# Kernel tuning notes

Hardware: AMD Instinct MI355X
Metric: run time of the kernel (lower is better)

## Reference

```python
import jax, jax.numpy as jnp
import numpy as np

B, T, D, H, FFN = 2, 2048, 1024, 16, 4096
K = D // H
EPS = 1e-6      # denominator clamp (module eps)
LN_EPS = 1e-5   # torch LayerNorm default
LAM_MIN = 1e-8  # lam clamp before log (exp(log(clamp)) == clamp)


def setup_inputs() -> dict:
    key = jax.random.key(0)
    ks = jax.random.split(key, 12)
    s = 0.02
    w = lambda k, shp: (jax.random.normal(k, shp, jnp.float32) * s)
    return {
        "x": jax.random.normal(ks[0], (B, T, D), jnp.float32),
        "q_w": w(ks[1], (D, D)), "q_b": jnp.zeros((D,), jnp.float32),
        "k_w": w(ks[2], (D, D)), "k_b": jnp.zeros((D,), jnp.float32),
        "v_w": w(ks[3], (D, D)), "v_b": jnp.zeros((D,), jnp.float32),
        "o_w": w(ks[4], (D, D)), "o_b": jnp.zeros((D,), jnp.float32),
        "ln1_w": jnp.ones((D,), jnp.float32), "ln1_b": jnp.zeros((D,), jnp.float32),
        "ln2_w": jnp.ones((D,), jnp.float32), "ln2_b": jnp.zeros((D,), jnp.float32),
        "dec_w": w(ks[5], (D, H)), "dec_b": jnp.full((H,), 5.0, jnp.float32),
        "f1_w": w(ks[6], (D, FFN)), "f1_b": jnp.zeros((FFN,), jnp.float32),
        "f2_w": w(ks[7], (FFN, D)), "f2_b": jnp.zeros((D,), jnp.float32),
    }


def _ln(x, w, b):
    m = x.mean(-1, keepdims=True)
    v = ((x - m) ** 2).mean(-1, keepdims=True)
    return (x - m) * jax.lax.rsqrt(v + LN_EPS) * w + b


def _lion(phi_q, phi_k, v, lam):
    """Bidirectional selective-decay linear attention.
    out_i = sum_j prod_{t in (min(i,j), max(i,j)]} lam_t * (phi_q_i . phi_k_j) v_j
    phi_q, phi_k, lam: (B,H,T,K); v: (B,H,T,Kv). Returns (B,H,T,Kv).
    Implemented as a forward scan (j<=i) + reverse scan (j>i); diagonal counted once.
    """
    b, h, t, kk = phi_q.shape
    kv = v.shape[-1]
    to_t = lambda a: a.transpose(2, 0, 1, 3)  # (T,B,H,*)
    qt, kt, vt, lt = to_t(phi_q), to_t(phi_k), to_t(v), to_t(lam)
    S0 = jnp.zeros((b, h, kk, kv), phi_q.dtype)

    def fwd(S, inp):
        q_t, k_t, v_t, l_t = inp
        S = S * l_t[..., None] + k_t[..., None] * v_t[..., None, :]
        return S, jnp.einsum('bhk,bhkv->bhv', q_t, S)

    _, out_f = jax.lax.scan(fwd, S0, (qt, kt, vt, lt))  # (T,B,H,Kv)

    q_shift = jnp.concatenate([qt[:1], qt[:-1]], axis=0)  # query at t-1 paired with R_{t-1}

    def bwd(R, inp):
        qs_t, k_t, v_t, l_t = inp
        R = l_t[..., None] * (k_t[..., None] * v_t[..., None, :] + R)
        return R, jnp.einsum('bhk,bhkv->bhv', qs_t, R)

    _, out_b = jax.lax.scan(bwd, S0, (q_shift, kt, vt, lt), reverse=True)
    # out_b[t] = phi_q_{t-1} . R_{t-1}; query i gets out_b[i+1]; R_{T-1} = 0
    out_b = jnp.concatenate([out_b[1:], jnp.zeros_like(out_b[:1])], axis=0)
    return (out_f + out_b).transpose(1, 2, 0, 3)  # (B,H,T,Kv)


def reference(x, q_w, q_b, k_w, k_b, v_w, v_b, o_w, o_b,
              ln1_w, ln1_b, ln2_w, ln2_b, dec_w, dec_b,
              f1_w, f1_b, f2_w, f2_b):
    bb, tt, dd = x.shape
    residual = x
    x_n = _ln(x, ln1_w, ln1_b)

    split = lambda y: y.reshape(bb, tt, H, K).transpose(0, 2, 1, 3)  # (B,H,T,K)
    q = split(x_n @ q_w + q_b)
    k = split(x_n @ k_w + k_b)
    v = split(x_n @ v_w + v_b)
    phi_q = jax.nn.elu(q) + 1.0
    phi_k = jax.nn.elu(k) + 1.0

    # selective per-head decay, broadcast across K
    lam = jax.nn.sigmoid(x_n @ dec_w + dec_b)            # (B,T,H)
    lam = jnp.maximum(lam, LAM_MIN).transpose(0, 2, 1)   # (B,H,T)
    lam = jnp.broadcast_to(lam[..., None], (bb, H, tt, K))

    # v-extended trick: extra ones column yields the row-sum denominator
    v_ext = jnp.concatenate([v, jnp.ones((bb, H, tt, 1), v.dtype)], axis=-1)
    out = _lion(phi_q, phi_k, v_ext, lam)                # (B,H,T,K+1)
    num, den = out[..., :K], jnp.maximum(out[..., K:], EPS)
    attn = (num / den).transpose(0, 2, 1, 3).reshape(bb, tt, dd)

    x = residual + (attn @ o_w + o_b)
    x2 = _ln(x, ln2_w, ln2_b)
    h = jax.nn.gelu(x2 @ f1_w + f1_b, approximate=False)
    return x + (h @ f2_w + f2_b)
```

## Files before the change

### kernel.cpp

```cpp
#include <hip/hip_runtime.h>
#include <cstdint>

#define Bq 2
#define Tq 2048
#define Dq 1024
#define Hq 16
#define FFNq 4096
#define NCHUNK 32
#define ROWS (Bq*Tq)
#define STW 5120

typedef unsigned short u16;
typedef __attribute__((ext_vector_type(4))) float f32x4;

enum { ACT_NONE = 0, ACT_ELU1 = 1, ACT_GELU = 2 };

#define MFMA16(acc, a, b) \
  asm("v_mfma_f32_16x16x32_bf16 %0, %1, %2, %0" : "+v"(acc) : "v"(a), "v"(b))
#define VMWAIT(N) asm volatile("s_waitcnt vmcnt(" #N ")" ::: "memory")

__device__ __forceinline__ u16 f2bf(float f) {
  uint32_t u = __float_as_uint(f);
  uint32_t r = (u + 0x7FFFu + ((u >> 16) & 1u)) >> 16;
  return (u16)r;
}
__device__ __forceinline__ float bf2f(u16 u) {
  return __uint_as_float(((uint32_t)u) << 16);
}

__device__ __forceinline__ void gload16(const void* g, void* l) {
  __builtin_amdgcn_global_load_lds(
      (const __attribute__((address_space(1))) uint32_t*)g,
      (__attribute__((address_space(3))) uint32_t*)l, 16, 0, 0);
}

__device__ __forceinline__ void xcd_swizzle(int& bx, int& by) {
  const int gx = gridDim.x;
  const int nwg = gx * gridDim.y;
  int flat = by * gx + bx;
  flat = (flat & 7) * (nwg >> 3) + (flat >> 3);
  bx = flat % gx;
  by = flat / gx;
}

__global__ __launch_bounds__(256) void wconv_all(
    const float* __restrict__ q_w, const float* __restrict__ k_w,
    const float* __restrict__ v_w, const float* __restrict__ o_w,
    const float* __restrict__ f1_w, const float* __restrict__ f2_w,
    u16* __restrict__ qkvT, u16* __restrict__ owT,
    u16* __restrict__ f1T, u16* __restrict__ f2T)
{
  const int bid = blockIdx.x;
  const float* src; u16* dst; int Kd, N, bx, by;
  if (bid < 1024) {
    const int m = bid >> 8, t = bid & 255;
    src = (m == 0) ? q_w : (m == 1) ? k_w : (m == 2) ? v_w : o_w;
    dst = (m == 3) ? owT : qkvT + (size_t)m * 1024 * 1024;
    Kd = 1024; N = 1024; bx = t & 15; by = t >> 4;
  } else if (bid < 2048) {
    const int t = bid - 1024;
    src = f1_w; dst = f1T; Kd = 1024; N = 4096; bx = t & 63; by = t >> 6;
  } else {
    const int t = bid - 2048;
    src = f2_w; dst = f2T; Kd = 4096; N = 1024; bx = t & 15; by = t >> 4;
  }
  __shared__ float tb[64][65];
  const int n0 = bx * 64, k0 = by * 64;
  const int tid = threadIdx.x;
  #pragma unroll
  for (int r = 0; r < 4; ++r) {
    const int s = tid + r * 256;
    const int kk = s >> 4, nn = (s & 15) << 2;
    const float4 v = *(const float4*)(src + (size_t)(k0 + kk) * N + n0 + nn);
    tb[kk][nn] = v.x; tb[kk][nn+1] = v.y; tb[kk][nn+2] = v.z; tb[kk][nn+3] = v.w;
  }
  __syncthreads();
  const int n = tid >> 2;
  const int ks = (tid & 3) << 4;
  uint32_t pk[8];
  #pragma unroll
  for (int j = 0; j < 8; ++j) {
    const float a = tb[ks + 2*j][n];
    const float c = tb[ks + 2*j + 1][n];
    pk[j] = (uint32_t)f2bf(a) | ((uint32_t)f2bf(c) << 16);
  }
  u16* drow = dst + (size_t)(n0 + n) * Kd + k0 + ks;
  *(uint4*)(drow)     = make_uint4(pk[0], pk[1], pk[2], pk[3]);
  *(uint4*)(drow + 8) = make_uint4(pk[4], pk[5], pk[6], pk[7]);
}

__global__ __launch_bounds__(256) void ln_kernel(
    const float* __restrict__ x, const float* __restrict__ w,
    const float* __restrict__ b, u16* __restrict__ outb)
{
  const int row = blockIdx.x;
  const int tid = threadIdx.x;
  const float* xr = x + (size_t)row * Dq;
  float4 v = *(const float4*)(xr + tid * 4);
  float s  = v.x + v.y + v.z + v.w;
  float s2 = v.x*v.x + v.y*v.y + v.z*v.z + v.w*v.w;
  #pragma unroll
  for (int off = 32; off > 0; off >>= 1) {
    s  += __shfl_down(s,  off);
    s2 += __shfl_down(s2, off);
  }
  __shared__ float rs[4], rs2[4];
  const int wid = tid >> 6, lane = tid & 63;
  if (lane == 0) { rs[wid] = s; rs2[wid] = s2; }
  __syncthreads();
  const float ts  = rs[0] + rs[1] + rs[2] + rs[3];
  const float ts2 = rs2[0] + rs2[1] + rs2[2] + rs2[3];
  const float mean = ts * (1.f / Dq);
  const float var  = ts2 * (1.f / Dq) - mean * mean;
  const float rstd = rsqrtf(var + 1e-5f);
  const float4 wv = *(const float4*)(w + tid * 4);
  const float4 bv = *(const float4*)(b + tid * 4);
  float4 o;
  o.x = (v.x - mean) * rstd * wv.x + bv.x;
  o.y = (v.y - mean) * rstd * wv.y + bv.y;
  o.z = (v.z - mean) * rstd * wv.z + bv.z;
  o.w = (v.w - mean) * rstd * wv.w + bv.w;
  uint2 p;
  p.x = (uint32_t)f2bf(o.x) | ((uint32_t)f2bf(o.y) << 16);
  p.y = (uint32_t)f2bf(o.z) | ((uint32_t)f2bf(o.w) << 16);
  *(uint2*)(outb + (size_t)row * Dq + tid * 4) = p;
}

template<int BM, int BN, int TW, int WM, int WN, int NB, int ACT, bool RES, bool F32OUT, bool QKVMODE>
__global__ __launch_bounds__(TW) void mgemm(
    const u16* __restrict__ A, const u16* __restrict__ BT,
    const float* __restrict__ b0, const float* __restrict__ b1,
    const float* __restrict__ b2, const float* __restrict__ res,
    void* __restrict__ C0, void* __restrict__ C1, void* __restrict__ C2,
    int M, int N, int Kd)
{
  constexpr int GA = (BM * 32) / (TW * 8);
  constexpr int GB = (BN * 32) / (TW * 8);
  constexpr int L  = GA + GB;
  constexpr int MR = BM / WM / 16;
  constexpr int NR = BN / WN / 16;
  constexpr int VMAIN = (NB - 2) * L;
  __shared__ u16 As[NB][BM * 32];
  __shared__ u16 Bs[NB][BN * 32];
  const int tid = threadIdx.x;
  const int lane = tid & 63, wid = tid >> 6;
  const int wr = wid / WN, wc = wid % WN;
  int bx = blockIdx.x, by = blockIdx.y;
  xcd_swizzle(bx, by);
  const int rowBase = by * BM;
  const int colBase = bx * BN;

  f32x4 acc[MR][NR] = {};

  const int srow = tid >> 2;
  const int skb  = (((tid & 3) ^ ((tid >> 3) & 3)) << 3);
  const u16* ag[GA];
  const u16* bg[GB];
  #pragma unroll
  for (int g = 0; g < GA; ++g)
    ag[g] = A  + (size_t)(rowBase + g * (TW / 4) + srow) * Kd + skb;
  #pragma unroll
  for (int g = 0; g < GB; ++g)
    bg[g] = BT + (size_t)(colBase + g * (TW / 4) + srow) * Kd + skb;

  const int fr = lane & 15, fq = lane >> 4;
  const int rsw = (fq ^ ((fr >> 1) & 3)) * 8;

  auto STAGE = [&](int buf, int k0) {
    #pragma unroll
    for (int g = 0; g < GA; ++g) gload16(ag[g] + k0, &As[buf][(g * TW + tid) * 8]);
    #pragma unroll
    for (int g = 0; g < GB; ++g) gload16(bg[g] + k0, &Bs[buf][(g * TW + tid) * 8]);
  };

  const int NT = Kd >> 5;
  #pragma unroll
  for (int s = 0; s < NB - 1; ++s) STAGE(s, s << 5);
  int cur = 0, wbuf = NB - 1;
  for (int t = 0; t < NT; ++t) {
    const int rem = NT - t;
    if (rem >= NB - 1) {
      if constexpr (VMAIN == 2)      VMWAIT(2);
      else if constexpr (VMAIN == 3) VMWAIT(3);
      else if constexpr (VMAIN == 4) VMWAIT(4);
      else if constexpr (VMAIN == 6) VMWAIT(6);
      else                           VMWAIT(8);
    } else if (NB >= 4 && rem == 2) {
      if constexpr (L == 2)      VMWAIT(2);
      else if constexpr (L == 3) VMWAIT(3);
      else                       VMWAIT(4);
    } else {
      VMWAIT(0);
    }
    __builtin_amdgcn_s_barrier();
    asm volatile("" ::: "memory");
    if (t + NB - 1 < NT) STAGE(wbuf, (t + NB - 1) << 5);
    f32x4 af[MR], bf_[NR];
    #pragma unroll
    for (int m = 0; m < MR; ++m)
      af[m] = *(const f32x4*)(&As[cur][(wr * (BM / WM) + m * 16 + fr) * 32 + rsw]);
    #pragma unroll
    for (int n = 0; n < NR; ++n)
      bf_[n] = *(const f32x4*)(&Bs[cur][(wc * (BN / WN) + n * 16 + fr) * 32 + rsw]);
    #pragma unroll
    for (int m = 0; m < MR; ++m)
      #pragma unroll
      for (int n = 0; n < NR; ++n)
        MFMA16(acc[m][n], af[m], bf_[n]);
    asm volatile("" ::: "memory");
    cur  = (cur  == NB - 1) ? 0 : cur + 1;
    wbuf = (wbuf == NB - 1) ? 0 : wbuf + 1;
  }

  if constexpr (QKVMODE) {
    const int wtype = colBase >> 10;
    const float* bp = (wtype == 0) ? b0 : (wtype == 1) ? b1 : b2;
    u16* outp = (u16*)((wtype == 0) ? C0 : (wtype == 1) ? C1 : C2);
    const int colB = colBase & 1023;
    #pragma unroll
    for (int m = 0; m < MR; ++m) {
      #pragma unroll
      for (int n = 0; n < NR; ++n) {
        const int col = colB + wc * (BN / WN) + n * 16 + fr;
        const float bv = bp[col];
        #pragma unroll
        for (int r = 0; r < 4; ++r) {
          const int row = rowBase + wr * (BM / WM) + m * 16 + fq * 4 + r;
          float val = acc[m][n][r] + bv;
          if (wtype < 2) val = (val >= 0.f) ? (val + 1.f) : expf(val);
          outp[(size_t)row * Dq + col] = f2bf(val);
        }
      }
    }
  } else {
    #pragma unroll
    for (int m = 0; m < MR; ++m) {
      #pragma unroll
      for (int n = 0; n < NR; ++n) {
        const int col = colBase + wc * (BN / WN) + n * 16 + fr;
        const float bv = b0[col];
        #pragma unroll
        for (int r = 0; r < 4; ++r) {
          const int row = rowBase + wr * (BM / WM) + m * 16 + fq * 4 + r;
          float val = acc[m][n][r] + bv;
          if (ACT == ACT_ELU1)      val = (val >= 0.f) ? (val + 1.f) : expf(val);
          else if (ACT == ACT_GELU) val = 0.5f * val * (1.f + erff(val * 0.70710678118f));
          if (RES) val += res[(size_t)row * N + col];
          if (F32OUT) ((float*)C0)[(size_t)row * N + col] = val;
          else        ((u16*)C0)[(size_t)row * N + col] = f2bf(val);
        }
      }
    }
  }
}

__global__ __launch_bounds__(256) void declam_kernel(
    const u16* __restrict__ xn, const float* __restrict__ dec_w,
    const float* __restrict__ dec_b, float* __restrict__ llam)
{
  const int row = blockIdx.x;
  const int tid = threadIdx.x;
  const int h = tid & 15, part = tid >> 4;
  const u16* xr = xn + (size_t)row * Dq;
  float s = 0.f;
  #pragma unroll 4
  for (int i = 0; i < 64; ++i) {
    const int d = part * 64 + i;
    s += bf2f(xr[d]) * dec_w[d * Hq + h];
  }
  __shared__ float ps[256];
  ps[tid] = s;
  __syncthreads();
  if (tid < 16) {
    float t = dec_b[tid];
    #pragma unroll
    for (int p = 0; p < 16; ++p) t += ps[p * 16 + tid];
    float lam = 1.f / (1.f + expf(-t));
    lam = fmaxf(lam, 1e-8f);
    llam[(size_t)row * Hq + tid] = logf(lam);
  }
}

__global__ __launch_bounds__(256) void lion_chunk_kernel(
    const u16* __restrict__ qb, const u16* __restrict__ kb,
    const u16* __restrict__ vb, const float* __restrict__ llam,
    u16* __restrict__ intra, u16* __restrict__ dS,
    u16* __restrict__ dR, float* __restrict__ lwout)
{
  const int c  = blockIdx.x;
  const int bh = blockIdx.y;
  const int b = bh >> 4, h = bh & 15;
  const int tid = threadIdx.x;
  const int lane = tid & 63, w = tid >> 6;
  const int fr = lane & 15, fq = lane >> 4;

  __shared__ __align__(16) u16 lds[37120];
  u16* qs   = lds;
  u16* ks   = lds + 5120;
  u16* vs   = lds + 10240;
  u16* kst1 = lds + 15360;
  u16* kst2 = lds + 20480;
  u16* v0t  = lds + 25600;
  u16* amt  = lds + 32000;
  u16* scr  = lds;
  __shared__ float lw[64], e1[64], e2[64];

  const size_t rowbase = ((size_t)(b * Tq + c * 64)) * Dq + h * 64;
  #pragma unroll
  for (int r = 0; r < 2; ++r) {
    const int s = tid + r * 256;
    const int u = s >> 3, e8 = (s & 7) << 3;
    *(uint4*)(&qs[u * 80 + e8]) = *(const uint4*)(qb + rowbase + (size_t)u * Dq + e8);
    *(uint4*)(&ks[u * 80 + e8]) = *(const uint4*)(kb + rowbase + (size_t)u * Dq + e8);
    *(uint4*)(&vs[u * 80 + e8]) = *(const uint4*)(vb + rowbase + (size_t)u * Dq + e8);
  }
  if (tid < 64) {
    const float lg = llam[((size_t)(b * Tq + c * 64 + tid)) * Hq + h];
    float sum = lg;
    #pragma unroll
    for (int off = 1; off < 64; off <<= 1) {
      const float y = __shfl_up(sum, off);
      if (tid >= off) sum += y;
    }
    lw[tid] = sum;
    const float lwE = __shfl(sum, 63);
    e1[tid] = expf(lwE - sum);
    e2[tid] = expf(sum);
    lwout[((size_t)bh * NCHUNK + c) * 64 + tid] = sum;
  }
  __syncthreads();

  for (int idx = tid; idx < 4096; idx += 256) {
    const int u = idx & 63, k = idx >> 6;
    const float kv_ = bf2f(ks[u * 80 + k]);
    kst1[k * 80 + u] = f2bf(e1[u] * kv_);
    kst2[k * 80 + u] = f2bf(e2[u] * kv_);
  }
  for (int idx = tid; idx < 6400; idx += 256) {
    const int u = idx & 63, kv = idx >> 6;
    u16 val;
    if (kv < 64)       val = vs[u * 80 + kv];
    else if (kv == 64) val = (u16)0x3F80;
    else               val = 0;
    v0t[kv * 80 + u] = val;
  }
  __syncthreads();

  {
    f32x4 qk[4] = {};
    #pragma unroll
    for (int s = 0; s < 2; ++s) {
      const f32x4 a = *(const f32x4*)(&qs[(16 * w + fr) * 80 + s * 32 + fq * 8]);
      #pragma unroll
      for (int n = 0; n < 4; ++n) {
        const f32x4 bb = *(const f32x4*)(&ks[(16 * n + fr) * 80 + s * 32 + fq * 8]);
        MFMA16(qk[n], a, bb);
      }
    }
    #pragma unroll
    for (int n = 0; n < 4; ++n) {
      const float lwj = lw[16 * n + fr];
      #pragma unroll
      for (int r = 0; r < 4; ++r) {
        const int row = 16 * w + fq * 4 + r;
        const float v = qk[n][r] * expf(-fabsf(lw[row] - lwj));
        amt[row * 80 + 16 * n + fr] = f2bf(v);
      }
    }
  }
  __syncthreads();

  const size_t ob = ((size_t)bh * NCHUNK + c) * (size_t)STW;

  {
    f32x4 acc5[5] = {};
    #pragma unroll
    for (int s = 0; s < 2; ++s) {
      const f32x4 a = *(const f32x4*)(&amt[(16 * w + fr) * 80 + s * 32 + fq * 8]);
      #pragma unroll
      for (int n = 0; n < 5; ++n) {
        const f32x4 bb = *(const f32x4*)(&v0t[(16 * n + fr) * 80 + s * 32 + fq * 8]);
        MFMA16(acc5[n], a, bb);
      }
    }
    #pragma unroll
    for (int n = 0; n < 5; ++n)
      #pragma unroll
      for (int r = 0; r < 4; ++r)
        intra[ob + (size_t)(16 * w + fq * 4 + r) * 80 + 16 * n + fr] = f2bf(acc5[n][r]);
  }

  {
    f32x4 acc5[5] = {};
    #pragma unroll
    for (int s = 0; s < 2; ++s) {
      const f32x4 a = *(const f32x4*)(&kst1[(16 * w + fr) * 80 + s * 32 + fq * 8]);
      #pragma unroll
      for (int n = 0; n < 5; ++n) {
        const f32x4 bb = *(const f32x4*)(&v0t[(16 * n + fr) * 80 + s * 32 + fq * 8]);
        MFMA16(acc5[n], a, bb);
      }
    }
    #pragma unroll
    for (int n = 0; n < 5; ++n)
      #pragma unroll
      for (int r = 0; r < 4; ++r)
        scr[(16 * n + fr) * 80 + (16 * w + fq * 4 + r)] = f2bf(acc5[n][r]);
  }
  __syncthreads();
  for (int i4 = tid; i4 < 640; i4 += 256) {
    const int kv = i4 >> 3, k8 = (i4 & 7) << 3;
    *(uint4*)(dS + ob + (size_t)kv * 64 + k8) = *(const uint4*)(&scr[kv * 80 + k8]);
  }
  __syncthreads();

  {
    f32x4 acc5[5] = {};
    #pragma unroll
    for (int s = 0; s < 2; ++s) {
      const f32x4 a = *(const f32x4*)(&kst2[(16 * w + fr) * 80 + s * 32 + fq * 8]);
      #pragma unroll
      for (int n = 0; n < 5; ++n) {
        const f32x4 bb = *(const f32x4*)(&v0t[(16 * n + fr) * 80 + s * 32 + fq * 8]);
        MFMA16(acc5[n], a, bb);
      }
    }
    #pragma unroll
    for (int n = 0; n < 5; ++n)
      #pragma unroll
      for (int r = 0; r < 4; ++r)
        scr[(16 * n + fr) * 80 + (16 * w + fq * 4 + r)] = f2bf(acc5[n][r]);
  }
  __syncthreads();
  for (int i4 = tid; i4 < 640; i4 += 256) {
    const int kv = i4 >> 3, k8 = (i4 & 7) << 3;
    *(uint4*)(dR + ob + (size_t)kv * 64 + k8) = *(const uint4*)(&scr[kv * 80 + k8]);
  }
}

__global__ __launch_bounds__(256) void lion_state_kernel(
    u16* __restrict__ dS, u16* __restrict__ dR,
    const float* __restrict__ lwbuf)
{
  const int bh  = blockIdx.y >> 1;
  const int dir = blockIdx.y & 1;
  const int e   = blockIdx.x * 256 + threadIdx.x;
  float st = 0.f;
  if (dir == 0) {
    for (int c = 0; c < NCHUNK; ++c) {
      const float d = expf(lwbuf[((size_t)bh * NCHUNK + c) * 64 + 63]);
      const size_t idx = ((size_t)bh * NCHUNK + c) * (size_t)STW + e;
      const float tmp = bf2f(dS[idx]);
      dS[idx] = f2bf(st);
      st = fmaf(d, st, tmp);
    }
  } else {
    for (int c = NCHUNK - 1; c >= 0; --c) {
      const float d = expf(lwbuf[((size_t)bh * NCHUNK + c) * 64 + 63]);
      const size_t idx = ((size_t)bh * NCHUNK + c) * (size_t)STW + e;
      const float tmp = bf2f(dR[idx]);
      dR[idx] = f2bf(st);
      st = fmaf(d, st, tmp);
    }
  }
}

__global__ __launch_bounds__(256) void lion_cross_kernel(
    const u16* __restrict__ qb, const u16* __restrict__ intra,
    const u16* __restrict__ Sst, const u16* __restrict__ Rst,
    const float* __restrict__ lwbuf, u16* __restrict__ attn)
{
  const int c  = blockIdx.x;
  const int bh = blockIdx.y;
  const int b = bh >> 4, h = bh & 15;
  const int tid = threadIdx.x;
  const int lane = tid & 63, w = tid >> 6;
  const int fr = lane & 15, fq = lane >> 4;

  __shared__ __align__(16) u16 ldsx[17920];
  u16* qs  = ldsx;
  u16* Stl = ldsx + 5120;
  u16* Rtl = ldsx + 11520;
  __shared__ float lw[64], den[64];

  const size_t rowbase = ((size_t)(b * Tq + c * 64)) * Dq + h * 64;
  const size_t ob = ((size_t)bh * NCHUNK + c) * (size_t)STW;
  #pragma unroll
  for (int r = 0; r < 2; ++r) {
    const int s = tid + r * 256;
    const int u = s >> 3, e8 = (s & 7) << 3;
    *(uint4*)(&qs[u * 80 + e8]) = *(const uint4*)(qb + rowbase + (size_t)u * Dq + e8);
  }
  for (int i4 = tid; i4 < 1280; i4 += 256) {
    const int hl = (i4 >= 640);
    const int j = hl ? i4 - 640 : i4;
    const int kv = j >> 3, k8 = (j & 7) << 3;
    const u16* srcp = (hl ? Rst : Sst) + ob + (size_t)kv * 64 + k8;
    u16* dstp = (hl ? Rtl : Stl) + kv * 80 + k8;
    *(uint4*)dstp = *(const uint4*)srcp;
  }
  if (tid < 64) lw[tid] = lwbuf[((size_t)bh * NCHUNK + c) * 64 + tid];
  __syncthreads();
  const float lwE = lw[63];

  f32x4 aS[5] = {}, aR[5] = {};
  #pragma unroll
  for (int s = 0; s < 2; ++s) {
    const f32x4 a = *(const f32x4*)(&qs[(16 * w + fr) * 80 + s * 32 + fq * 8]);
    #pragma unroll
    for (int n = 0; n < 5; ++n) {
      const f32x4 sb = *(const f32x4*)(&Stl[(16 * n + fr) * 80 + s * 32 + fq * 8]);
      const f32x4 rb = *(const f32x4*)(&Rtl[(16 * n + fr) * 80 + s * 32 + fq * 8]);
      MFMA16(aS[n], a, sb);
      MFMA16(aR[n], a, rb);
    }
  }

  float outv[5][4];
  float efr[4], ebr[4];
  #pragma unroll
  for (int r = 0; r < 4; ++r) {
    const int row = 16 * w + fq * 4 + r;
    efr[r] = expf(lw[row]);
    ebr[r] = expf(lwE - lw[row]);
  }
  #pragma unroll
  for (int n = 0; n < 5; ++n)
    #pragma unroll
    for (int r = 0; r < 4; ++r) {
      const int row = 16 * w + fq * 4 + r;
      outv[n][r] = bf2f(intra[ob + (size_t)row * 80 + 16 * n + fr])
                 + efr[r] * aS[n][r] + ebr[r] * aR[n][r];
    }
  if (fr == 0) {
    #pragma unroll
    for (int r = 0; r < 4; ++r) den[16 * w + fq * 4 + r] = outv[4][r];
  }
  __syncthreads();
  #pragma unroll
  for (int n = 0; n < 4; ++n)
    #pragma unroll
    for (int r = 0; r < 4; ++r) {
      const int row = 16 * w + fq * 4 + r;
      const float dv = fmaxf(den[row], 1e-6f);
      attn[rowbase + (size_t)row * Dq + 16 * n + fr] = f2bf(outv[n][r] / dv);
    }
}

extern "C" void kernel_launch(void* const* d_in, const int* in_sizes, int n_in,
                              void* d_out, int out_size, void* d_ws, size_t ws_size,
                              hipStream_t stream)
{
  const float* x     = (const float*)d_in[0];
  const float* q_w   = (const float*)d_in[1];
  const float* q_b   = (const float*)d_in[2];
  const float* k_w   = (const float*)d_in[3];
  const float* k_b   = (const float*)d_in[4];
  const float* v_w   = (const float*)d_in[5];
  const float* v_b   = (const float*)d_in[6];
  const float* o_w   = (const float*)d_in[7];
  const float* o_b   = (const float*)d_in[8];
  const float* ln1_w = (const float*)d_in[9];
  const float* ln1_b = (const float*)d_in[10];
  const float* ln2_w = (const float*)d_in[11];
  const float* ln2_b = (const float*)d_in[12];
  const float* dec_w = (const float*)d_in[13];
  const float* dec_b = (const float*)d_in[14];
  const float* f1_w  = (const float*)d_in[15];
  const float* f1_b  = (const float*)d_in[16];
  const float* f2_w  = (const float*)d_in[17];
  const float* f2_b  = (const float*)d_in[18];
  float* out = (float*)d_out;
  float* ws  = (float*)d_ws;

  size_t o = 0;
  float* xa    = ws + o; o += (size_t)ROWS * Dq;
  u16*   xnb   = (u16*)(ws + o); o += (size_t)ROWS * Dq / 2;
  u16*   qbuf  = (u16*)(ws + o); o += (size_t)ROWS * Dq / 2;
  u16*   kbuf  = (u16*)(ws + o); o += (size_t)ROWS * Dq / 2;
  u16*   vbuf  = (u16*)(ws + o); o += (size_t)ROWS * Dq / 2;
  u16*   attnb = (u16*)(ws + o); o += (size_t)ROWS * Dq / 2;
  u16*   hb    = qbuf;
  float* llam  = ws + o; o += (size_t)ROWS * Hq;
  float* lwb   = ws + o; o += (size_t)32 * NCHUNK * 64;
  u16*   dSt   = (u16*)(ws + o); o += (size_t)32 * NCHUNK * STW / 2;
  u16*   dRt   = (u16*)(ws + o); o += (size_t)32 * NCHUNK * STW / 2;
  u16*   intrab= (u16*)(ws + o); o += (size_t)32 * NCHUNK * STW / 2;
  u16*   x2b   = intrab;
  u16*   qkvT  = (u16*)(ws + o); o += (size_t)3 * Dq * Dq / 2;
  u16*   owT   = (u16*)(ws + o); o += (size_t)Dq * Dq / 2;
  u16*   f1T   = (u16*)(ws + o); o += (size_t)Dq * FFNq / 2;
  u16*   f2T   = (u16*)(ws + o); o += (size_t)Dq * FFNq / 2;

  wconv_all<<<3072, 256, 0, stream>>>(q_w, k_w, v_w, o_w, f1_w, f2_w,
                                      qkvT, owT, f1T, f2T);

  ln_kernel<<<ROWS, 256, 0, stream>>>(x, ln1_w, ln1_b, xnb);
  mgemm<128, 128, 256, 2, 2, 3, ACT_NONE, false, false, true><<<dim3(24, 32), 256, 0, stream>>>(
      xnb, qkvT, q_b, k_b, v_b, nullptr, qbuf, kbuf, vbuf, ROWS, 3072, Dq);
  declam_kernel<<<ROWS, 256, 0, stream>>>(xnb, dec_w, dec_b, llam);

  lion_chunk_kernel<<<dim3(NCHUNK, 32), 256, 0, stream>>>(qbuf, kbuf, vbuf, llam, intrab, dSt, dRt, lwb);
  lion_state_kernel<<<dim3(20, 64), 256, 0, stream>>>(dSt, dRt, lwb);
  lion_cross_kernel<<<dim3(NCHUNK, 32), 256, 0, stream>>>(qbuf, intrab, dSt, dRt, lwb, attnb);

  mgemm<64, 64, 256, 2, 2, 4, ACT_NONE, true, true, false><<<dim3(16, 64), 256, 0, stream>>>(
      attnb, owT, o_b, nullptr, nullptr, x, xa, nullptr, nullptr, ROWS, Dq, Dq);
  ln_kernel<<<ROWS, 256, 0, stream>>>(xa, ln2_w, ln2_b, x2b);
  mgemm<256, 256, 512, 2, 4, 3, ACT_GELU, false, false, false><<<dim3(16, 16), 512, 0, stream>>>(
      x2b, f1T, f1_b, nullptr, nullptr, nullptr, hb, nullptr, nullptr, ROWS, FFNq, Dq);
  mgemm<64, 64, 256, 2, 2, 4, ACT_NONE, true, true, false><<<dim3(16, 64), 256, 0, stream>>>(
      hb, f2T, f2_b, nullptr, nullptr, xa, out, nullptr, nullptr, ROWS, Dq, FFNq);
}
```

Before: 273.4 us.

## Split-K the second FFN GEMM with larger tiles and a separate reduce kernel

The FFN down-projection GEMM changes from 64x64 tiles over the full K=4096 to 128x128 tiles with K split in two. Each split writes bf16 partial sums into reused workspace. A new elementwise kernel then adds the two partials, the bias and the residual into the fp32 output. The aim is more data reuse per tile while keeping enough workgroups to fill the GPU. The cost is an extra launch, extra global traffic for the partials, and extra rounding from storing partials in bf16.

```diff
diff --git a/kernel.cpp b/kernel.cpp
--- a/kernel.cpp
+++ b/kernel.cpp
@@ -27,6 +27,8 @@
 __device__ __forceinline__ float bf2f(u16 u) {
   return __uint_as_float(((uint32_t)u) << 16);
 }
+__device__ __forceinline__ float bflo(uint32_t w) { return __uint_as_float(w << 16); }
+__device__ __forceinline__ float bfhi(uint32_t w) { return __uint_as_float(w & 0xffff0000u); }
 
 __device__ __forceinline__ void gload16(const void* g, void* l) {
   __builtin_amdgcn_global_load_lds(
@@ -126,7 +128,7 @@
   *(uint2*)(outb + (size_t)row * Dq + tid * 4) = p;
 }
 
-template<int BM, int BN, int TW, int WM, int WN, int NB, int ACT, bool RES, bool F32OUT, bool QKVMODE>
+template<int BM, int BN, int TW, int WM, int WN, int NB, int SK, int ACT, bool RES, bool F32OUT, bool QKVMODE>
 __global__ __launch_bounds__(TW) void mgemm(
     const u16* __restrict__ A, const u16* __restrict__ BT,
     const float* __restrict__ b0, const float* __restrict__ b1,
@@ -149,6 +151,8 @@
   xcd_swizzle(bx, by);
   const int rowBase = by * BM;
   const int colBase = bx * BN;
+  const int bz  = (SK > 1) ? (int)blockIdx.z : 0;
+  const int kb0 = bz * (Kd / SK);
 
   f32x4 acc[MR][NR] = {};
 
@@ -158,10 +162,10 @@
   const u16* bg[GB];
   #pragma unroll
   for (int g = 0; g < GA; ++g)
-    ag[g] = A  + (size_t)(rowBase + g * (TW / 4) + srow) * Kd + skb;
+    ag[g] = A  + (size_t)(rowBase + g * (TW / 4) + srow) * Kd + kb0 + skb;
   #pragma unroll
   for (int g = 0; g < GB; ++g)
-    bg[g] = BT + (size_t)(colBase + g * (TW / 4) + srow) * Kd + skb;
+    bg[g] = BT + (size_t)(colBase + g * (TW / 4) + srow) * Kd + kb0 + skb;
 
   const int fr = lane & 15, fq = lane >> 4;
   const int rsw = (fq ^ ((fr >> 1) & 3)) * 8;
@@ -173,7 +177,7 @@
     for (int g = 0; g < GB; ++g) gload16(bg[g] + k0, &Bs[buf][(g * TW + tid) * 8]);
   };
 
-  const int NT = Kd >> 5;
+  const int NT = (Kd / SK) >> 5;
   #pragma unroll
   for (int s = 0; s < NB - 1; ++s) STAGE(s, s << 5);
   int cur = 0, wbuf = NB - 1;
@@ -212,7 +216,21 @@
     wbuf = (wbuf == NB - 1) ? 0 : wbuf + 1;
   }
 
-  if constexpr (QKVMODE) {
+  if constexpr (SK > 1) {
+    u16* pp = (u16*)C1 + (size_t)bz * ((size_t)M * N);
+    #pragma unroll
+    for (int m = 0; m < MR; ++m) {
+      #pragma unroll
+      for (int n = 0; n < NR; ++n) {
+        const int col = colBase + wc * (BN / WN) + n * 16 + fr;
+        #pragma unroll
+        for (int r = 0; r < 4; ++r) {
+          const int row = rowBase + wr * (BM / WM) + m * 16 + fq * 4 + r;
+          pp[(size_t)row * N + col] = f2bf(acc[m][n][r]);
+        }
+      }
+    }
+  } else if constexpr (QKVMODE) {
     const int wtype = colBase >> 10;
     const float* bp = (wtype == 0) ? b0 : (wtype == 1) ? b1 : b2;
     u16* outp = (u16*)((wtype == 0) ? C0 : (wtype == 1) ? C1 : C2);
@@ -252,6 +270,34 @@
       }
     }
   }
+}
+
+__global__ __launch_bounds__(256) void ffn2_reduce(
+    const u16* __restrict__ p, const float* __restrict__ bias,
+    const float* __restrict__ res, float* __restrict__ out)
+{
+  const size_t base = ((size_t)blockIdx.x * 256 + threadIdx.x) * 8;
+  const size_t MN = (size_t)ROWS * Dq;
+  const uint4 a0 = *(const uint4*)(p + base);
+  const uint4 a1 = *(const uint4*)(p + MN + base);
+  const int col = (int)(base & (Dq - 1));
+  float r[8];
+  const uint32_t w0[4] = {a0.x, a0.y, a0.z, a0.w};
+  const uint32_t w1[4] = {a1.x, a1.y, a1.z, a1.w};
+  #pragma unroll
+  for (int j = 0; j < 4; ++j) {
+    r[2*j]   = bflo(w0[j]) + bflo(w1[j]);
+    r[2*j+1] = bfhi(w0[j]) + bfhi(w1[j]);
+  }
+  const float4 x0 = *(const float4*)(res + base);
+  const float4 x1 = *(const float4*)(res + base + 4);
+  float4 o0, o1;
+  o0.x = r[0] + bias[col+0] + x0.x;  o0.y = r[1] + bias[col+1] + x0.y;
+  o0.z = r[2] + bias[col+2] + x0.z;  o0.w = r[3] + bias[col+3] + x0.w;
+  o1.x = r[4] + bias[col+4] + x1.x;  o1.y = r[5] + bias[col+5] + x1.y;
+  o1.z = r[6] + bias[col+6] + x1.z;  o1.w = r[7] + bias[col+7] + x1.w;
+  *(float4*)(out + base)     = o0;
+  *(float4*)(out + base + 4) = o1;
 }
 
 __global__ __launch_bounds__(256) void declam_kernel(
@@ -585,6 +631,7 @@
   float* lwb   = ws + o; o += (size_t)32 * NCHUNK * 64;
   u16*   dSt   = (u16*)(ws + o); o += (size_t)32 * NCHUNK * STW / 2;
   u16*   dRt   = (u16*)(ws + o); o += (size_t)32 * NCHUNK * STW / 2;
+  u16*   pker  = dSt;
   u16*   intrab= (u16*)(ws + o); o += (size_t)32 * NCHUNK * STW / 2;
   u16*   x2b   = intrab;
   u16*   qkvT  = (u16*)(ws + o); o += (size_t)3 * Dq * Dq / 2;
@@ -596,7 +643,7 @@
                                       qkvT, owT, f1T, f2T);
 
   ln_kernel<<<ROWS, 256, 0, stream>>>(x, ln1_w, ln1_b, xnb);
-  mgemm<128, 128, 256, 2, 2, 3, ACT_NONE, false, false, true><<<dim3(24, 32), 256, 0, stream>>>(
+  mgemm<128, 128, 256, 2, 2, 3, 1, ACT_NONE, false, false, true><<<dim3(24, 32), 256, 0, stream>>>(
       xnb, qkvT, q_b, k_b, v_b, nullptr, qbuf, kbuf, vbuf, ROWS, 3072, Dq);
   declam_kernel<<<ROWS, 256, 0, stream>>>(xnb, dec_w, dec_b, llam);
 
@@ -604,11 +651,12 @@
   lion_state_kernel<<<dim3(20, 64), 256, 0, stream>>>(dSt, dRt, lwb);
   lion_cross_kernel<<<dim3(NCHUNK, 32), 256, 0, stream>>>(qbuf, intrab, dSt, dRt, lwb, attnb);
 
-  mgemm<64, 64, 256, 2, 2, 4, ACT_NONE, true, true, false><<<dim3(16, 64), 256, 0, stream>>>(
+  mgemm<64, 64, 256, 2, 2, 4, 1, ACT_NONE, true, true, false><<<dim3(16, 64), 256, 0, stream>>>(
       attnb, owT, o_b, nullptr, nullptr, x, xa, nullptr, nullptr, ROWS, Dq, Dq);
   ln_kernel<<<ROWS, 256, 0, stream>>>(xa, ln2_w, ln2_b, x2b);
-  mgemm<256, 256, 512, 2, 4, 3, ACT_GELU, false, false, false><<<dim3(16, 16), 512, 0, stream>>>(
+  mgemm<256, 256, 512, 2, 4, 3, 1, ACT_GELU, false, false, false><<<dim3(16, 16), 512, 0, stream>>>(
       x2b, f1T, f1_b, nullptr, nullptr, nullptr, hb, nullptr, nullptr, ROWS, FFNq, Dq);
-  mgemm<64, 64, 256, 2, 2, 4, ACT_NONE, true, true, false><<<dim3(16, 64), 256, 0, stream>>>(
-      hb, f2T, f2_b, nullptr, nullptr, xa, out, nullptr, nullptr, ROWS, Dq, FFNq);
-}
+  mgemm<128, 128, 256, 2, 2, 3, 2, ACT_NONE, false, false, false><<<dim3(8, 32, 2), 256, 0, stream>>>(
+      hb, f2T, f2_b, nullptr, nullptr, nullptr, nullptr, pker, nullptr, ROWS, Dq, FFNq);
+  ffn2_reduce<<<2048, 256, 0, stream>>>(pker, f2_b, xa, out);
+}
```

After: 266.2 us, median of 2. 1.03x faster.
